# Performance work log

Measured on AMD Instinct MI355X. Metric: run time of the kernel, lower is better.

Reference implementation:

```python
import jax, jax.numpy as jnp
import numpy as np

N = 8192
E = 262144
F_IN, H1, H2 = 512, 256, 128


def setup_inputs() -> dict:
    key = jax.random.key(0)
    ks = jax.random.split(key, 7)
    x = jax.random.normal(ks[0], (N, F_IN), dtype=jnp.float32)
    # glorot-ish init scale
    W1 = jax.random.normal(ks[1], (F_IN, H1), dtype=jnp.float32) * (1.0 / np.sqrt(F_IN))
    W2 = jax.random.normal(ks[2], (H1, H2), dtype=jnp.float32) * (1.0 / np.sqrt(H1))
    W3 = jax.random.normal(ks[3], (H1, H2), dtype=jnp.float32) * (1.0 / np.sqrt(H1))
    edge_w = jax.random.uniform(ks[4], (E,), dtype=jnp.float32) / 32.0  # ~normalized adj
    row = jax.random.randint(ks[5], (E,), 0, N, dtype=jnp.int64)
    col = jax.random.randint(ks[6], (E,), 0, N, dtype=jnp.int64)
    return {"x": x, "W1": W1, "W2": W2, "W3": W3, "edge_w": edge_w, "row": row, "col": col}


def _spmm(row, col, edge_w, h):
    # sparse adjacency aggregate: out[i] = sum_{e: row[e]==i} edge_w[e] * h[col[e]]
    msgs = edge_w[:, None] * h[col]  # [E, d]
    return jax.ops.segment_sum(msgs, row, num_segments=N)


def reference(x, W1, W2, W3, edge_w, row, col):
    # gc1: dropout(off, eval) -> matmul -> spmm -> relu
    h1 = jax.nn.relu(_spmm(row, col, edge_w, x @ W1))  # [N, H1]
    # gc2 / gc3: identity activation
    mu = _spmm(row, col, edge_w, h1 @ W2)              # [N, H2]
    logvar = _spmm(row, col, edge_w, h1 @ W3)          # [N, H2]
    z = mu  # eval-mode reparameterize returns mu
    adj_rec = z @ z.T  # [N, N], decoder act = identity
    return (h1, adj_rec, mu, logvar, z)
```

## Files before the change

kernel.cpp:

```cpp
#include <hip/hip_runtime.h>

typedef __bf16 bf16_t;
typedef __bf16 bf16x4 __attribute__((ext_vector_type(4)));
typedef __bf16 bf16x8 __attribute__((ext_vector_type(8)));
typedef float floatx4 __attribute__((ext_vector_type(4)));

static constexpr int NN  = 8192;
static constexpr int FIN = 512;
static constexpr int NH1 = 256;
static constexpr int NH2 = 128;
static constexpr int NE  = 262144;

static constexpr size_t OFF_H1     = 0;
static constexpr size_t OFF_ADJ    = (size_t)NN * NH1;
static constexpr size_t OFF_MU     = OFF_ADJ + (size_t)NN * NN;
static constexpr size_t OFF_LOGVAR = OFF_MU + (size_t)NN * NH2;
static constexpr size_t OFF_Z      = OFF_LOGVAR + (size_t)NN * NH2;

__global__ __launch_bounds__(256) void prep_all(
    const float* __restrict__ W1, const float* __restrict__ W2,
    const float* __restrict__ W3, const int* __restrict__ row,
    bf16_t* __restrict__ W1T, bf16_t* __restrict__ W23T,
    int* __restrict__ counts) {
  const int gid = blockIdx.x * 256 + threadIdx.x;
  atomicAdd(&counts[row[gid]], 1);
  if (gid < NH1 * FIN) {
    const int n = gid >> 9, k = gid & 511;
    W1T[gid] = (bf16_t)W1[k * NH1 + n];
  }
  if (gid < NH1 * NH1) {
    const int n = gid >> 8, k = gid & 255;
    W23T[gid] = (bf16_t)(n < NH2 ? W2[k * NH2 + n] : W3[k * NH2 + (n - NH2)]);
  }
}

__global__ __launch_bounds__(1024) void scan8k(const int* __restrict__ counts,
                                               int* __restrict__ row_ptr) {
  __shared__ int part[1024];
  const int t = threadIdx.x;
  int v[8];
  int run = 0;
#pragma unroll
  for (int j = 0; j < 8; ++j) { run += counts[t * 8 + j]; v[j] = run; }
  part[t] = run;
  __syncthreads();
  for (int off = 1; off < 1024; off <<= 1) {
    const int x = (t >= off) ? part[t - off] : 0;
    __syncthreads();
    part[t] += x;
    __syncthreads();
  }
  const int base = (t > 0) ? part[t - 1] : 0;
#pragma unroll
  for (int j = 0; j < 8; ++j) row_ptr[t * 8 + j + 1] = base + v[j];
  if (t == 0) row_ptr[0] = 0;
}

__global__ __launch_bounds__(256) void edge_fill(
    const int* __restrict__ row, const int* __restrict__ col,
    const float* __restrict__ edge_w, const int* __restrict__ row_ptr,
    int* __restrict__ cursor, uint2* __restrict__ pw) {
  const int e = blockIdx.x * 256 + threadIdx.x;
  const int r = row[e];
  const int p = atomicAdd(&cursor[r], 1);
  uint2 v;
  v.x = (unsigned)col[e];
  v.y = __float_as_uint(edge_w[e]);
  pw[row_ptr[r] + p] = v;
}

template <int KD, int RT, bool ABF, int EPI, bool SWZ>
__global__ __launch_bounds__(256) void mfma_gemm(
    const float* __restrict__ Af, const bf16_t* __restrict__ Abf,
    const bf16_t* __restrict__ BT, float* __restrict__ C, int ldc,
    float* __restrict__ dout, bf16_t* __restrict__ zbf, int ldz) {
  int bx, by;
  if constexpr (SWZ) {
    const int bid = blockIdx.x;
    const int s = (bid & 7) * 512 + (bid >> 3);
    by = s >> 6; bx = s & 63;
  } else {
    bx = blockIdx.x; by = blockIdx.y;
  }
  const int lane = threadIdx.x & 63;
  const int wid  = threadIdx.x >> 6;
  const int l15  = lane & 15;
  const int lg   = lane >> 4;
  const int brow = by * (RT * 32) + (wid >> 1) * (RT * 16);
  const int bcol = bx * 128 + (wid & 1) * 64;

  floatx4 acc[RT][4];
#pragma unroll
  for (int i = 0; i < RT; ++i)
#pragma unroll
    for (int j = 0; j < 4; ++j) acc[i][j] = (floatx4){0.f, 0.f, 0.f, 0.f};

#pragma unroll 1
  for (int kk = 0; kk < KD; kk += 32) {
    bf16x8 a[RT], b[4];
#pragma unroll
    for (int rt = 0; rt < RT; ++rt) {
      const int r = brow + rt * 16 + l15;
      if constexpr (ABF) {
        a[rt] = *(const bf16x8*)(Abf + (size_t)r * KD + kk + lg * 8);
      } else {
        const float* p = Af + (size_t)r * KD + kk + lg * 8;
        const floatx4 lo = *(const floatx4*)p;
        const floatx4 hi = *(const floatx4*)(p + 4);
        bf16x8 t;
        t[0] = (bf16_t)lo[0]; t[1] = (bf16_t)lo[1];
        t[2] = (bf16_t)lo[2]; t[3] = (bf16_t)lo[3];
        t[4] = (bf16_t)hi[0]; t[5] = (bf16_t)hi[1];
        t[6] = (bf16_t)hi[2]; t[7] = (bf16_t)hi[3];
        a[rt] = t;
      }
    }
#pragma unroll
    for (int ct = 0; ct < 4; ++ct) {
      const int c = bcol + ct * 16 + l15;
      b[ct] = *(const bf16x8*)(BT + (size_t)c * KD + kk + lg * 8);
    }
#pragma unroll
    for (int rt = 0; rt < RT; ++rt)
#pragma unroll
      for (int ct = 0; ct < 4; ++ct)
        acc[rt][ct] = __builtin_amdgcn_mfma_f32_16x16x32_bf16(
            a[rt], b[ct], acc[rt][ct], 0, 0, 0);
  }

  __shared__ float lt[4][16 * 68];
  float* L = lt[wid];
#pragma unroll
  for (int rt = 0; rt < RT; ++rt) {
#pragma unroll
    for (int ct = 0; ct < 4; ++ct)
#pragma unroll
      for (int r = 0; r < 4; ++r)
        L[(lg * 4 + r) * 68 + ct * 16 + l15] = acc[rt][ct][r];
    __builtin_amdgcn_wave_barrier();
#pragma unroll
    for (int it = 0; it < 4; ++it) {
      const int idx = it * 64 + lane;
      const int rr = idx >> 4, c4 = idx & 15;
      const floatx4 v = *(const floatx4*)(L + rr * 68 + c4 * 4);
      const int orow = brow + rt * 16 + rr;
      const int gc = bcol + c4 * 4;
      if constexpr (EPI == 0) {
        __builtin_nontemporal_store(v, (floatx4*)(C + (size_t)orow * ldc + gc));
      } else if constexpr (EPI == 1) {
        if (gc < NH2) {
          __builtin_nontemporal_store(
              v, (floatx4*)(dout + OFF_MU + (size_t)orow * NH2 + gc));
          __builtin_nontemporal_store(
              v, (floatx4*)(dout + OFF_Z + (size_t)orow * NH2 + gc));
          bf16x4 o;
          o[0] = (bf16_t)v[0]; o[1] = (bf16_t)v[1];
          o[2] = (bf16_t)v[2]; o[3] = (bf16_t)v[3];
          *(bf16x4*)(zbf + (size_t)orow * ldz + gc) = o;
        } else {
          __builtin_nontemporal_store(
              v, (floatx4*)(dout + OFF_LOGVAR + (size_t)orow * NH2 + gc - NH2));
        }
      } else {
        bf16x4 o;
        o[0] = (bf16_t)v[0]; o[1] = (bf16_t)v[1];
        o[2] = (bf16_t)v[2]; o[3] = (bf16_t)v[3];
        *(bf16x4*)(zbf + (size_t)orow * ldz + gc) = o;
      }
    }
    __builtin_amdgcn_wave_barrier();
  }
}

template <bool RELU>
__global__ __launch_bounds__(256) void spmm_b(
    const int* __restrict__ row_ptr, const uint2* __restrict__ pw,
    const bf16_t* __restrict__ src, float* __restrict__ dst_f,
    bf16_t* __restrict__ dst_b) {
  const int lane = threadIdx.x & 63;
  const int r = blockIdx.x * 4 + (threadIdx.x >> 6);
  const int li = lane & 15;
  const int g  = lane >> 4;
  const int beg = row_ptr[r];
  const int end = row_ptr[r + 1];
  float acc[16];
#pragma unroll
  for (int c = 0; c < 16; ++c) acc[c] = 0.f;

  for (int base = beg; base < end; base += 64) {
    const int t = base + lane;
    uint2 cw;
    cw.x = 0; cw.y = 0;
    if (t < end) cw = pw[t];
    const int cnt = min(64, end - base);
#pragma unroll 2
    for (int j4 = 0; j4 < cnt; j4 += 4) {
      const int cj = __shfl((int)cw.x, j4 + g);
      const float wj = __shfl(__uint_as_float(cw.y), j4 + g);
      const bf16_t* p = src + (size_t)cj * NH1 + li * 16;
      const bf16x8 v0 = *(const bf16x8*)p;
      const bf16x8 v1 = *(const bf16x8*)(p + 8);
#pragma unroll
      for (int c = 0; c < 8; ++c) {
        acc[c]     += wj * (float)v0[c];
        acc[8 + c] += wj * (float)v1[c];
      }
    }
  }
#pragma unroll
  for (int c = 0; c < 16; ++c) {
    acc[c] += __shfl_xor(acc[c], 16);
    acc[c] += __shfl_xor(acc[c], 32);
    if constexpr (RELU) acc[c] = fmaxf(acc[c], 0.f);
  }
  float o0, o1, o2, o3;
  switch (g) {
    case 0:  o0 = acc[0];  o1 = acc[1];  o2 = acc[2];  o3 = acc[3];  break;
    case 1:  o0 = acc[4];  o1 = acc[5];  o2 = acc[6];  o3 = acc[7];  break;
    case 2:  o0 = acc[8];  o1 = acc[9];  o2 = acc[10]; o3 = acc[11]; break;
    default: o0 = acc[12]; o1 = acc[13]; o2 = acc[14]; o3 = acc[15]; break;
  }
  const int ch = li * 16 + g * 4;
  if (dst_f) {
    floatx4 o = (floatx4){o0, o1, o2, o3};
    __builtin_nontemporal_store(o, (floatx4*)(dst_f + (size_t)r * NH1 + ch));
  }
  if (dst_b) {
    bf16x4 o;
    o[0] = (bf16_t)o0; o[1] = (bf16_t)o1; o[2] = (bf16_t)o2; o[3] = (bf16_t)o3;
    *(bf16x4*)(dst_b + (size_t)r * NH1 + ch) = o;
  }
}

extern "C" void kernel_launch(void* const* d_in, const int* in_sizes, int n_in,
                              void* d_out, int out_size, void* d_ws, size_t ws_size,
                              hipStream_t stream) {
  const float* x      = (const float*)d_in[0];
  const float* W1     = (const float*)d_in[1];
  const float* W2     = (const float*)d_in[2];
  const float* W3     = (const float*)d_in[3];
  const float* edge_w = (const float*)d_in[4];
  const int*   row    = (const int*)d_in[5];
  const int*   col    = (const int*)d_in[6];
  float* out = (float*)d_out;
  char*  ws  = (char*)d_ws;

  bf16_t* XWb  = (bf16_t*)(ws);
  bf16_t* h1b  = (bf16_t*)(ws + (4u << 20));
  bf16_t* gb   = (bf16_t*)(ws + (8u << 20));
  bf16_t* zbf  = (bf16_t*)(ws + (12u << 20));
  bf16_t* W1T  = (bf16_t*)(ws + (14u << 20));
  bf16_t* W23T = (bf16_t*)(ws + (14u << 20) + (1u << 19));
  int* counts   = (int*)(ws + (15u << 20));
  int* cursor   = counts + NN;
  int* row_ptr  = cursor + NN;
  uint2* pw     = (uint2*)(ws + (15u << 20) + (1u << 18));

  hipMemsetAsync(counts, 0, 2 * NN * sizeof(int), stream);
  prep_all<<<NE / 256, 256, 0, stream>>>(W1, W2, W3, row, W1T, W23T, counts);
  scan8k<<<1, 1024, 0, stream>>>(counts, row_ptr);
  edge_fill<<<NE / 256, 256, 0, stream>>>(row, col, edge_w, row_ptr, cursor, pw);

  mfma_gemm<FIN, 2, false, 2, false><<<dim3(NH1 / 128, NN / 64), 256, 0, stream>>>(
      x, nullptr, W1T, nullptr, 0, nullptr, XWb, NH1);
  spmm_b<true><<<NN / 4, 256, 0, stream>>>(row_ptr, pw, XWb, out + OFF_H1, h1b);
  spmm_b<false><<<NN / 4, 256, 0, stream>>>(row_ptr, pw, h1b, nullptr, gb);
  mfma_gemm<NH1, 2, true, 1, false><<<dim3(NH1 / 128, NN / 64), 256, 0, stream>>>(
      nullptr, gb, W23T, nullptr, 0, out, zbf, NH2);
  mfma_gemm<NH2, 4, true, 0, true><<<4096, 256, 0, stream>>>(
      nullptr, zbf, zbf, out + OFF_ADJ, NN, nullptr, nullptr, 0);
}
```

Measured before the change: 158.5 us.

## Replace CSR build with fixed-capacity row buckets fused into the first GEMM

Drops the memset, count, prefix-scan and fill kernels that built CSR. Each edge now atomically claims a slot in a per-row bucket of capacity 128, and overflow edges go to a spill list that the SpMM scans linearly. The edge bucketing runs as extra blocks inside the same launch as the x@W1 GEMM, which overlaps the two and removes several serial launches. The cost is a larger, sparsely filled bucket array with worse locality. A heavily skewed degree distribution would also hit the slow spill path.

```diff
diff --git a/kernel.cpp b/kernel.cpp
--- a/kernel.cpp
+++ b/kernel.cpp
@@ -10,6 +10,7 @@
 static constexpr int NH1 = 256;
 static constexpr int NH2 = 128;
 static constexpr int NE  = 262144;
+static constexpr int CAP = 128;
 
 static constexpr size_t OFF_H1     = 0;
 static constexpr size_t OFF_ADJ    = (size_t)NN * NH1;
@@ -17,75 +18,14 @@
 static constexpr size_t OFF_LOGVAR = OFF_MU + (size_t)NN * NH2;
 static constexpr size_t OFF_Z      = OFF_LOGVAR + (size_t)NN * NH2;
 
-__global__ __launch_bounds__(256) void prep_all(
-    const float* __restrict__ W1, const float* __restrict__ W2,
-    const float* __restrict__ W3, const int* __restrict__ row,
-    bf16_t* __restrict__ W1T, bf16_t* __restrict__ W23T,
-    int* __restrict__ counts) {
-  const int gid = blockIdx.x * 256 + threadIdx.x;
-  atomicAdd(&counts[row[gid]], 1);
-  if (gid < NH1 * FIN) {
-    const int n = gid >> 9, k = gid & 511;
-    W1T[gid] = (bf16_t)W1[k * NH1 + n];
-  }
-  if (gid < NH1 * NH1) {
-    const int n = gid >> 8, k = gid & 255;
-    W23T[gid] = (bf16_t)(n < NH2 ? W2[k * NH2 + n] : W3[k * NH2 + (n - NH2)]);
-  }
-}
-
-__global__ __launch_bounds__(1024) void scan8k(const int* __restrict__ counts,
-                                               int* __restrict__ row_ptr) {
-  __shared__ int part[1024];
-  const int t = threadIdx.x;
-  int v[8];
-  int run = 0;
-#pragma unroll
-  for (int j = 0; j < 8; ++j) { run += counts[t * 8 + j]; v[j] = run; }
-  part[t] = run;
-  __syncthreads();
-  for (int off = 1; off < 1024; off <<= 1) {
-    const int x = (t >= off) ? part[t - off] : 0;
-    __syncthreads();
-    part[t] += x;
-    __syncthreads();
-  }
-  const int base = (t > 0) ? part[t - 1] : 0;
-#pragma unroll
-  for (int j = 0; j < 8; ++j) row_ptr[t * 8 + j + 1] = base + v[j];
-  if (t == 0) row_ptr[0] = 0;
-}
-
-__global__ __launch_bounds__(256) void edge_fill(
-    const int* __restrict__ row, const int* __restrict__ col,
-    const float* __restrict__ edge_w, const int* __restrict__ row_ptr,
-    int* __restrict__ cursor, uint2* __restrict__ pw) {
-  const int e = blockIdx.x * 256 + threadIdx.x;
-  const int r = row[e];
-  const int p = atomicAdd(&cursor[r], 1);
-  uint2 v;
-  v.x = (unsigned)col[e];
-  v.y = __float_as_uint(edge_w[e]);
-  pw[row_ptr[r] + p] = v;
-}
-
-template <int KD, int RT, bool ABF, int EPI, bool SWZ>
-__global__ __launch_bounds__(256) void mfma_gemm(
-    const float* __restrict__ Af, const bf16_t* __restrict__ Abf,
+template <int KD, int RT, bool ABF, int EPI>
+__device__ __forceinline__ void gemm_body(
+    int bx, int by, const float* __restrict__ Af, const bf16_t* __restrict__ Abf,
     const bf16_t* __restrict__ BT, float* __restrict__ C, int ldc,
-    float* __restrict__ dout, bf16_t* __restrict__ zbf, int ldz) {
-  int bx, by;
-  if constexpr (SWZ) {
-    const int bid = blockIdx.x;
-    const int s = (bid & 7) * 512 + (bid >> 3);
-    by = s >> 6; bx = s & 63;
-  } else {
-    bx = blockIdx.x; by = blockIdx.y;
-  }
-  const int lane = threadIdx.x & 63;
-  const int wid  = threadIdx.x >> 6;
-  const int l15  = lane & 15;
-  const int lg   = lane >> 4;
+    float* __restrict__ dout, bf16_t* __restrict__ zb, int ldz,
+    float* __restrict__ L, int lane, int wid) {
+  const int l15 = lane & 15;
+  const int lg  = lane >> 4;
   const int brow = by * (RT * 32) + (wid >> 1) * (RT * 16);
   const int bcol = bx * 128 + (wid & 1) * 64;
 
@@ -128,8 +68,6 @@
             a[rt], b[ct], acc[rt][ct], 0, 0, 0);
   }
 
-  __shared__ float lt[4][16 * 68];
-  float* L = lt[wid];
 #pragma unroll
   for (int rt = 0; rt < RT; ++rt) {
 #pragma unroll
@@ -156,7 +94,7 @@
           bf16x4 o;
           o[0] = (bf16_t)v[0]; o[1] = (bf16_t)v[1];
           o[2] = (bf16_t)v[2]; o[3] = (bf16_t)v[3];
-          *(bf16x4*)(zbf + (size_t)orow * ldz + gc) = o;
+          *(bf16x4*)(zb + (size_t)orow * ldz + gc) = o;
         } else {
           __builtin_nontemporal_store(
               v, (floatx4*)(dout + OFF_LOGVAR + (size_t)orow * NH2 + gc - NH2));
@@ -165,34 +103,81 @@
         bf16x4 o;
         o[0] = (bf16_t)v[0]; o[1] = (bf16_t)v[1];
         o[2] = (bf16_t)v[2]; o[3] = (bf16_t)v[3];
-        *(bf16x4*)(zbf + (size_t)orow * ldz + gc) = o;
+        *(bf16x4*)(zb + (size_t)orow * ldz + gc) = o;
       }
     }
     __builtin_amdgcn_wave_barrier();
   }
 }
 
+__global__ __launch_bounds__(256) void k_prep(
+    const float* __restrict__ W1, const float* __restrict__ W2,
+    const float* __restrict__ W3, bf16_t* __restrict__ W1T,
+    bf16_t* __restrict__ W23T, int* __restrict__ counts) {
+  const int gid = blockIdx.x * 256 + threadIdx.x;
+  if (gid <= NN) counts[gid] = 0;
+  if (gid < NH1 * FIN) {
+    const int n = gid >> 9, k = gid & 511;
+    W1T[gid] = (bf16_t)W1[k * NH1 + n];
+  }
+  if (gid < NH1 * NH1) {
+    const int n = gid >> 8, k = gid & 255;
+    W23T[gid] = (bf16_t)(n < NH2 ? W2[k * NH2 + n] : W3[k * NH2 + (n - NH2)]);
+  }
+}
+
+__global__ __launch_bounds__(256) void k_fat(
+    const float* __restrict__ x, const bf16_t* __restrict__ W1T,
+    bf16_t* __restrict__ XWb, const int* __restrict__ row,
+    const int* __restrict__ col, const float* __restrict__ edge_w,
+    int* __restrict__ counts, uint2* __restrict__ bucket,
+    uint4* __restrict__ spill) {
+  __shared__ float lt[4][16 * 68];
+  const int bid = blockIdx.x;
+  if (bid < 256) {
+    const int lane = threadIdx.x & 63;
+    const int wid  = threadIdx.x >> 6;
+    gemm_body<FIN, 2, false, 2>(bid & 1, bid >> 1, x, nullptr, W1T, nullptr, 0,
+                                nullptr, XWb, NH1, lt[wid], lane, wid);
+  } else {
+    const int e = (bid - 256) * 256 + threadIdx.x;
+    const int r = row[e];
+    const int p = atomicAdd(&counts[r], 1);
+    if (p < CAP) {
+      uint2 v;
+      v.x = (unsigned)col[e];
+      v.y = __float_as_uint(edge_w[e]);
+      bucket[(size_t)r * CAP + p] = v;
+    } else {
+      const int s = atomicAdd(&counts[NN], 1);
+      uint4 v;
+      v.x = (unsigned)r; v.y = (unsigned)col[e];
+      v.z = __float_as_uint(edge_w[e]); v.w = 0;
+      spill[s] = v;
+    }
+  }
+}
+
 template <bool RELU>
-__global__ __launch_bounds__(256) void spmm_b(
-    const int* __restrict__ row_ptr, const uint2* __restrict__ pw,
-    const bf16_t* __restrict__ src, float* __restrict__ dst_f,
-    bf16_t* __restrict__ dst_b) {
+__global__ __launch_bounds__(256) void spmm_bucket(
+    const int* __restrict__ counts, const uint2* __restrict__ bucket,
+    const uint4* __restrict__ spill, const bf16_t* __restrict__ src,
+    float* __restrict__ dst_f, bf16_t* __restrict__ dst_b) {
   const int lane = threadIdx.x & 63;
   const int r = blockIdx.x * 4 + (threadIdx.x >> 6);
   const int li = lane & 15;
   const int g  = lane >> 4;
-  const int beg = row_ptr[r];
-  const int end = row_ptr[r + 1];
+  const int deg = min(counts[r], CAP);
   float acc[16];
 #pragma unroll
   for (int c = 0; c < 16; ++c) acc[c] = 0.f;
 
-  for (int base = beg; base < end; base += 64) {
+  for (int base = 0; base < deg; base += 64) {
     const int t = base + lane;
     uint2 cw;
     cw.x = 0; cw.y = 0;
-    if (t < end) cw = pw[t];
-    const int cnt = min(64, end - base);
+    if (t < deg) cw = bucket[(size_t)r * CAP + t];
+    const int cnt = min(64, deg - base);
 #pragma unroll 2
     for (int j4 = 0; j4 < cnt; j4 += 4) {
       const int cj = __shfl((int)cw.x, j4 + g);
@@ -207,6 +192,23 @@
       }
     }
   }
+  const int ns = counts[NN];
+  if (ns > 0 && g == 0) {
+    for (int i = 0; i < ns; ++i) {
+      const uint4 s = spill[i];
+      if ((int)s.x == r) {
+        const float wj = __uint_as_float(s.z);
+        const bf16_t* p = src + (size_t)s.y * NH1 + li * 16;
+        const bf16x8 v0 = *(const bf16x8*)p;
+        const bf16x8 v1 = *(const bf16x8*)(p + 8);
+#pragma unroll
+        for (int c = 0; c < 8; ++c) {
+          acc[c]     += wj * (float)v0[c];
+          acc[8 + c] += wj * (float)v1[c];
+        }
+      }
+    }
+  }
 #pragma unroll
   for (int c = 0; c < 16; ++c) {
     acc[c] += __shfl_xor(acc[c], 16);
@@ -230,6 +232,26 @@
     o[0] = (bf16_t)o0; o[1] = (bf16_t)o1; o[2] = (bf16_t)o2; o[3] = (bf16_t)o3;
     *(bf16x4*)(dst_b + (size_t)r * NH1 + ch) = o;
   }
+}
+
+template <int KD, int RT, bool ABF, int EPI, bool SWZ>
+__global__ __launch_bounds__(256) void mfma_gemm(
+    const float* __restrict__ Af, const bf16_t* __restrict__ Abf,
+    const bf16_t* __restrict__ BT, float* __restrict__ C, int ldc,
+    float* __restrict__ dout, bf16_t* __restrict__ zb, int ldz) {
+  __shared__ float lt[4][16 * 68];
+  int bx, by;
+  if constexpr (SWZ) {
+    const int bid = blockIdx.x;
+    const int s = (bid & 7) * 512 + (bid >> 3);
+    by = s >> 6; bx = s & 63;
+  } else {
+    bx = blockIdx.x; by = blockIdx.y;
+  }
+  const int lane = threadIdx.x & 63;
+  const int wid  = threadIdx.x >> 6;
+  gemm_body<KD, RT, ABF, EPI>(bx, by, Af, Abf, BT, C, ldc, dout, zb, ldz,
+                              lt[wid], lane, wid);
 }
 
 extern "C" void kernel_launch(void* const* d_in, const int* in_sizes, int n_in,
@@ -247,25 +269,22 @@
 
   bf16_t* XWb  = (bf16_t*)(ws);
   bf16_t* h1b  = (bf16_t*)(ws + (4u << 20));
-  bf16_t* gb   = (bf16_t*)(ws + (8u << 20));
-  bf16_t* zbf  = (bf16_t*)(ws + (12u << 20));
-  bf16_t* W1T  = (bf16_t*)(ws + (14u << 20));
-  bf16_t* W23T = (bf16_t*)(ws + (14u << 20) + (1u << 19));
-  int* counts   = (int*)(ws + (15u << 20));
-  int* cursor   = counts + NN;
-  int* row_ptr  = cursor + NN;
-  uint2* pw     = (uint2*)(ws + (15u << 20) + (1u << 18));
-
-  hipMemsetAsync(counts, 0, 2 * NN * sizeof(int), stream);
-  prep_all<<<NE / 256, 256, 0, stream>>>(W1, W2, W3, row, W1T, W23T, counts);
-  scan8k<<<1, 1024, 0, stream>>>(counts, row_ptr);
-  edge_fill<<<NE / 256, 256, 0, stream>>>(row, col, edge_w, row_ptr, cursor, pw);
-
-  mfma_gemm<FIN, 2, false, 2, false><<<dim3(NH1 / 128, NN / 64), 256, 0, stream>>>(
-      x, nullptr, W1T, nullptr, 0, nullptr, XWb, NH1);
-  spmm_b<true><<<NN / 4, 256, 0, stream>>>(row_ptr, pw, XWb, out + OFF_H1, h1b);
-  spmm_b<false><<<NN / 4, 256, 0, stream>>>(row_ptr, pw, h1b, nullptr, gb);
-  mfma_gemm<NH1, 2, true, 1, false><<<dim3(NH1 / 128, NN / 64), 256, 0, stream>>>(
+  bf16_t* W1T  = (bf16_t*)(ws + (8u << 20));
+  bf16_t* W23T = (bf16_t*)(ws + (8u << 20) + (1u << 18));
+  int*    counts = (int*)(ws + (8u << 20) + (3u << 18));
+  uint2*  bucket = (uint2*)(ws + (9u << 20));
+  uint4*  spill  = (uint4*)(ws + (17u << 20));
+  bf16_t* gb  = XWb;
+  bf16_t* zbf = h1b;
+
+  k_prep<<<512, 256, 0, stream>>>(W1, W2, W3, W1T, W23T, counts);
+  k_fat<<<1280, 256, 0, stream>>>(x, W1T, XWb, row, col, edge_w, counts, bucket,
+                                  spill);
+  spmm_bucket<true><<<NN / 4, 256, 0, stream>>>(counts, bucket, spill, XWb,
+                                                out + OFF_H1, h1b);
+  spmm_bucket<false><<<NN / 4, 256, 0, stream>>>(counts, bucket, spill, h1b,
+                                                 nullptr, gb);
+  mfma_gemm<NH1, 2, true, 1, false><<<dim3(2, 128), 256, 0, stream>>>(
       nullptr, gb, W23T, nullptr, 0, out, zbf, NH2);
   mfma_gemm<NH2, 4, true, 0, true><<<4096, 256, 0, stream>>>(
       nullptr, zbf, zbf, out + OFF_ADJ, NN, nullptr, nullptr, 0);
```

After: 141.2 us. 10.9% less time.
